# Kernel optimization log

Measured on AMD Instinct MI355X. Metric: run time of the kernel, lower is better.

## Reference

```python
import jax, jax.numpy as jnp
import numpy as np

B, P, EPG = 1000, 100, 1200  # graphs, nodes/graph, edges/graph
IN, HID, OUT, K = 16, 64, 5, 3


def setup_inputs() -> dict:
    key = jax.random.key(0)
    ks = jax.random.split(key, 12)
    offs = jnp.repeat(jnp.arange(B, dtype=jnp.int32) * P, EPG)
    src = jax.random.randint(ks[0], (B * EPG,), 0, P, dtype=jnp.int32) + offs
    dst = jax.random.randint(ks[1], (B * EPG,), 0, P, dtype=jnp.int32) + offs
    graph_ids = jnp.repeat(jnp.arange(B, dtype=jnp.int32), P)
    feat = jax.random.normal(ks[2], (B * P, IN), dtype=jnp.float32)

    def lin(k1, fan_in, fan_out):
        s = 1.0 / np.sqrt(fan_in)
        return jax.random.uniform(k1, (fan_in, fan_out), jnp.float32, -s, s)

    return {
        'feat': feat, 'src': src, 'dst': dst, 'graph_ids': graph_ids,
        'n_graphs': B,
        'W1': lin(ks[3], K * IN, HID), 'b1': jnp.zeros((HID,), jnp.float32),
        'W2': lin(ks[4], K * HID, HID), 'b2': jnp.zeros((HID,), jnp.float32),
        'W3': lin(ks[5], K * HID, HID), 'b3': jnp.zeros((HID,), jnp.float32),
        'Wfc': lin(ks[6], HID, OUT), 'bfc': jnp.zeros((OUT,), jnp.float32),
    }


def _cheb_conv(x, src, dst, d_invsqrt, W, b, k):
    # DGL ChebConv with lambda_max=2 -> re_norm=1, scaled Laplacian = -D^-1/2 A D^-1/2
    n = x.shape[0]

    def Ax(h):
        msg = (h * d_invsqrt)[src]                      # gather from source nodes
        agg = jax.ops.segment_sum(msg, dst, num_segments=n)
        return agg * d_invsqrt

    Xs = [x]
    if k > 1:
        Xs.append(-Ax(Xs[0]))                           # X1 = L_hat X0
        for _ in range(2, k):
            Xs.append(-2.0 * Ax(Xs[-1]) - Xs[-2])       # X_i = 2 L_hat X_{i-1} - X_{i-2}
    Xt = jnp.concatenate(Xs, axis=1)                    # [n, k*f]
    return Xt @ W + b


def reference(feat, src, dst, graph_ids, n_graphs, W1, b1, W2, b2, W3, b3, Wfc, bfc):
    n = feat.shape[0]
    deg = jax.ops.segment_sum(jnp.ones((src.shape[0],), feat.dtype), dst, num_segments=n)
    d_invsqrt = jnp.where(deg < 1.0, 1.0, deg) ** -0.5
    d_invsqrt = d_invsqrt[:, None]

    h = jax.nn.relu(_cheb_conv(feat, src, dst, d_invsqrt, W1, b1, K))
    h = jax.nn.relu(_cheb_conv(h, src, dst, d_invsqrt, W2, b2, K))
    h = jax.nn.relu(_cheb_conv(h, src, dst, d_invsqrt, W3, b3, K))

    # dgl.mean_nodes: per-graph mean pooling
    counts = jax.ops.segment_sum(jnp.ones((n,), h.dtype), graph_ids, num_segments=n_graphs)
    hg = jax.ops.segment_sum(h, graph_ids, num_segments=n_graphs) / counts[:, None]
    return hg @ Wfc + bfc
```

## Files before the change

kernel.cpp:

```cpp
#include <hip/hip_runtime.h>

#define NGRAPH 1000
#define P      100
#define EPG    1200
#define INF    16
#define HID    64
#define NOUT   5


#define FSTR   96
#define T1OFF  64
#define T2OFF  80

#define RK1 64
#define RK2 208
#define L1HI 0
#define L1LO 4096
#define L2HI 8192
#define L2LO 21504
#define L3HI 34816
#define L3LO 48128

typedef short short8 __attribute__((ext_vector_type(8)));
typedef float f32x4  __attribute__((ext_vector_type(4)));

__device__ __forceinline__ int swf(int row, int col) {
    return row * FSTR + (col ^ (((row >> 3) & 3) << 3));
}

__device__ __forceinline__ unsigned packsplit(float x) {
    unsigned u  = __float_as_uint(x);
    unsigned hi = (u + 0x7fffu + ((u >> 16) & 1u)) >> 16;
    float r = x - __uint_as_float(hi << 16);
    unsigned v  = __float_as_uint(r);
    unsigned lo = (v + 0x7fffu + ((v >> 16) & 1u)) >> 16;
    return (hi << 16) | (lo & 0xffffu);
}

__device__ __forceinline__ float up2(short h, short l) {
    return __uint_as_float(((unsigned)(unsigned short)h) << 16) +
           __uint_as_float(((unsigned)(unsigned short)l) << 16);
}

__global__ __launch_bounds__(256) void wprep(
    const float* __restrict__ W1, const float* __restrict__ W2,
    const float* __restrict__ W3, short* __restrict__ wt)
{
    const int i0 = blockIdx.x * blockDim.x + threadIdx.x;
    const int stride = gridDim.x * blockDim.x;
    for (int e = i0; e < HID * RK1; e += stride) {
        int c = e / RK1, r = e % RK1;
        float v = (r < 3 * INF) ? W1[r * HID + c] : 0.f;
        unsigned p = packsplit(v);
        wt[L1HI + e] = (short)(p >> 16);
        wt[L1LO + e] = (short)(p & 0xffffu);
    }
    for (int e = i0; e < HID * RK2; e += stride) {
        int c = e / RK2, r = e % RK2;
        float v2 = (r < 3 * HID) ? W2[r * HID + c] : 0.f;
        float v3 = (r < 3 * HID) ? W3[r * HID + c] : 0.f;
        unsigned p2 = packsplit(v2), p3 = packsplit(v3);
        wt[L2HI + e] = (short)(p2 >> 16); wt[L2LO + e] = (short)(p2 & 0xffffu);
        wt[L3HI + e] = (short)(p3 >> 16); wt[L3LO + e] = (short)(p3 & 0xffffu);
    }
}

template <int SECOND>
__device__ __forceinline__ void dense_prop(
    short* __restrict__ Ahi, short* __restrict__ Alo,
    short8 a00, short8 a01, short8 a02, short8 a03,
    short8 a10, short8 a11, short8 a12, short8 a13,
    bool has2, int srcoff, int dstoff, int ycb,
    int rb0, int rb1, f32x4 dv0, f32x4 dv1, int lane)
{
    const int n16 = lane & 15;
    const int q   = lane >> 4;
    const int kq  = q * 8;
    const int c = (srcoff + n16) ^ (q << 3);
    f32x4 p0, p1;
    p0[0]=0.f; p0[1]=0.f; p0[2]=0.f; p0[3]=0.f;
    p1[0]=0.f; p1[1]=0.f; p1[2]=0.f; p1[3]=0.f;

#define PROPK(KK, A0, A1) { \
    const int b0 = (KK * 32 + kq) * FSTR + c; \
    short8 bhi, blo; \
    if (KK < 3) { \
        bhi[0]=Ahi[b0        ]; blo[0]=Alo[b0        ]; \
        bhi[1]=Ahi[b0+1*FSTR ]; blo[1]=Alo[b0+1*FSTR ]; \
        bhi[2]=Ahi[b0+2*FSTR ]; blo[2]=Alo[b0+2*FSTR ]; \
        bhi[3]=Ahi[b0+3*FSTR ]; blo[3]=Alo[b0+3*FSTR ]; \
        bhi[4]=Ahi[b0+4*FSTR ]; blo[4]=Alo[b0+4*FSTR ]; \
        bhi[5]=Ahi[b0+5*FSTR ]; blo[5]=Alo[b0+5*FSTR ]; \
        bhi[6]=Ahi[b0+6*FSTR ]; blo[6]=Alo[b0+6*FSTR ]; \
        bhi[7]=Ahi[b0+7*FSTR ]; blo[7]=Alo[b0+7*FSTR ]; \
    } else { \
        const int m0 = 96 + kq; \
        const int i0 = (m0+0 < P ? (m0+0)*FSTR : 0) + c; \
        const int i1 = (m0+1 < P ? (m0+1)*FSTR : 0) + c; \
        const int i2 = (m0+2 < P ? (m0+2)*FSTR : 0) + c; \
        const int i3 = (m0+3 < P ? (m0+3)*FSTR : 0) + c; \
        bhi[0]=Ahi[i0]; blo[0]=Alo[i0]; \
        bhi[1]=Ahi[i1]; blo[1]=Alo[i1]; \
        bhi[2]=Ahi[i2]; blo[2]=Alo[i2]; \
        bhi[3]=Ahi[i3]; blo[3]=Alo[i3]; \
        bhi[4]=0; blo[4]=0; \
        bhi[5]=0; blo[5]=0; \
        bhi[6]=0; blo[6]=0; \
        bhi[7]=0; blo[7]=0; \
    } \
    p0 = __builtin_amdgcn_mfma_f32_16x16x32_bf16(A0, bhi, p0, 0, 0, 0); \
    p0 = __builtin_amdgcn_mfma_f32_16x16x32_bf16(A0, blo, p0, 0, 0, 0); \
    if (has2) { \
        p1 = __builtin_amdgcn_mfma_f32_16x16x32_bf16(A1, bhi, p1, 0, 0, 0); \
        p1 = __builtin_amdgcn_mfma_f32_16x16x32_bf16(A1, blo, p1, 0, 0, 0); \
    } }

    PROPK(0, a00, a10)
    PROPK(1, a01, a11)
    PROPK(2, a02, a12)
    PROPK(3, a03, a13)
#undef PROPK

#pragma unroll
    for (int r = 0; r < 4; r++) {
        const int row = rb0 + q * 4 + r;
        const float d2 = dv0[r] * dv0[r];
        float o;
        if (SECOND) {
            const int yi = swf(row, ycb + n16);
            o = -2.f * d2 * p0[r] - up2(Ahi[yi], Alo[yi]);
        } else o = -d2 * p0[r];
        const int di = swf(row, dstoff + n16);
        const unsigned pp = packsplit(o);
        Ahi[di] = (short)(pp >> 16); Alo[di] = (short)pp;
    }
    if (has2) {
#pragma unroll
        for (int r = 0; r < 4; r++) {
            const int row = rb1 + q * 4 + r;
            if (rb1 != 84 || row >= 96) {
                const float d2 = dv1[r] * dv1[r];
                float o;
                if (SECOND) {
                    const int yi = swf(row, ycb + n16);
                    o = -2.f * d2 * p1[r] - up2(Ahi[yi], Alo[yi]);
                } else o = -d2 * p1[r];
                const int di = swf(row, dstoff + n16);
                const unsigned pp = packsplit(o);
                Ahi[di] = (short)(pp >> 16); Alo[di] = (short)pp;
            }
        }
    }
}

template <int F, int FINAL>
__device__ __forceinline__ void cheb_layer(
    short* __restrict__ Ahi, short* __restrict__ Alo,
    const float* __restrict__ dinv,
    short8 a00, short8 a01, short8 a02, short8 a03,
    short8 a10, short8 a11, short8 a12, short8 a13, bool has2,
    const short* __restrict__ whi, const short* __restrict__ wlo,
    const float* __restrict__ bias,
    int tid, int rb0, int rb1, f32x4 dv0, f32x4 dv1)
{
    const int RK   = 3 * F + 16;
    const int lane = tid & 63;
    const int wv   = tid >> 6;
    const int n16  = lane & 15;
    const int q    = lane >> 4;
    const int ncol = (wv << 4) + n16;

    f32x4 acc[7];
#pragma unroll
    for (int t = 0; t < 7; t++) { acc[t][0]=0.f; acc[t][1]=0.f; acc[t][2]=0.f; acc[t][3]=0.f; }

    for (int cb = 0; cb < F; cb += 16) {
        dense_prop<0>(Ahi, Alo, a00,a01,a02,a03, a10,a11,a12,a13, has2,
                      cb,    T1OFF, 0,  rb0, rb1, dv0, dv1, lane);
        __syncthreads();
        dense_prop<1>(Ahi, Alo, a00,a01,a02,a03, a10,a11,a12,a13, has2,
                      T1OFF, T2OFF, cb, rb0, rb1, dv0, dv1, lane);
        __syncthreads();

#pragma unroll
        for (int ks = 0; ks < 2; ks++) {
            int wr, aoff;
            if (ks == 0) {
                wr   = (q == 0) ? cb : (q == 1) ? cb + 8 : (q == 2) ? F + cb : F + cb + 8;
                aoff = (q == 0) ? cb : (q == 1) ? cb + 8 : (q == 2) ? T1OFF  : T1OFF + 8;
            } else {
                wr   = (q == 0) ? 2*F + cb : (q == 1) ? 2*F + cb + 8 : (q == 2) ? 3*F : 3*F + 8;
                aoff = (q == 0) ? T2OFF    : (q == 1) ? T2OFF + 8    : (q == 2) ? T1OFF : T1OFF + 8;
            }
            const short8 bhi = *(const short8*)&whi[ncol * RK + wr];
            const short8 blo = *(const short8*)&wlo[ncol * RK + wr];
#pragma unroll
            for (int t = 0; t < 7; t++) {
                const int row = ((t < 6) ? t * 16 : 84) + n16;
                const int ax  = row * FSTR + (aoff ^ (((row >> 3) & 3) << 3));
                const short8 ahi = *(const short8*)&Ahi[ax];
                const short8 alo = *(const short8*)&Alo[ax];
                acc[t] = __builtin_amdgcn_mfma_f32_16x16x32_bf16(ahi, bhi, acc[t], 0, 0, 0);
                acc[t] = __builtin_amdgcn_mfma_f32_16x16x32_bf16(ahi, blo, acc[t], 0, 0, 0);
                acc[t] = __builtin_amdgcn_mfma_f32_16x16x32_bf16(alo, bhi, acc[t], 0, 0, 0);
            }
        }
        __syncthreads();
    }

    const float bcol = bias[ncol];
#pragma unroll
    for (int t = 0; t < 7; t++) {
        const int rbase = ((t < 6) ? t * 16 : 84) + q * 4;
#pragma unroll
        for (int r = 0; r < 4; r++) {
            const int row = rbase + r;
            if (t < 6 || row >= 96) {
                const float dn = dinv[row];
                const float v = acc[t][r];
                float o;
                if (FINAL) o = fmaxf(v * (1.0f / dn) + bcol, 0.f);
                else       o = fmaxf(v + bcol * dn, 0.f);
                const int oi = swf(row, ncol);
                const unsigned pp = packsplit(o);
                Ahi[oi] = (short)(pp >> 16); Alo[oi] = (short)pp;
            }
        }
    }
    __syncthreads();
}

__global__ __launch_bounds__(256, 4) void gnn_kernel(
    const float* __restrict__ feat,
    const int* __restrict__ src, const int* __restrict__ dst,
    const float* __restrict__ b1, const float* __restrict__ b2,
    const float* __restrict__ b3,
    const float* __restrict__ Wfc, const float* __restrict__ bfc,
    const short* __restrict__ wt,
    float* __restrict__ out)
{
    __shared__ __align__(16) unsigned ldsu[9728];
    __shared__ float meta[128];
    short* Ahi = (short*)ldsu;
    short* Alo = (short*)ldsu + 9600;
    unsigned* cnt = ldsu;

    const int g = blockIdx.x;
    const int tid = threadIdx.x;
    const int base = g * P;
    const int* srcg = src + g * EPG;
    const int* dstg = dst + g * EPG;

    int* deg = (int*)meta;
    for (int i = tid; i < 6400; i += 256) cnt[i] = 0u;
    for (int i = tid; i < P; i += 256) deg[i] = 0;
    __syncthreads();
    for (int e = tid; e < EPG; e += 256) {
        int s = srcg[e] - base;
        int d = dstg[e] - base;
        atomicAdd(&deg[d], 1);
        atomicAdd(&cnt[d * 64 + (s >> 1)], 1u << ((s & 1) * 16));
    }
    __syncthreads();
    for (int i = tid; i < P; i += 256) {
        int dg = deg[i];
        meta[i] = rsqrtf((float)(dg > 1 ? dg : 1));
    }
    const int lane = tid & 63, wv = tid >> 6, q = lane >> 4, n16 = lane & 15;
    const int rb0 = wv * 16;
    const int t2i = wv + 4;
    const int rb1 = (t2i >= 6) ? 84 : t2i * 16;
    const bool has2 = (wv < 3);
    const int arow0 = rb0 + n16;
    const int arow1 = (has2 ? rb1 : rb0) + n16;
    short8 a00, a01, a02, a03, a10, a11, a12, a13;
#define MKA(VAR, AR, KK) { \
    const unsigned w0 = cnt[(AR) * 64 + (KK) * 16 + q * 4 + 0]; \
    const unsigned w1 = cnt[(AR) * 64 + (KK) * 16 + q * 4 + 1]; \
    const unsigned w2 = cnt[(AR) * 64 + (KK) * 16 + q * 4 + 2]; \
    const unsigned w3 = cnt[(AR) * 64 + (KK) * 16 + q * 4 + 3]; \
    short8 t; \
    t[0] = (short)(__float_as_uint((float)(w0 & 0xffffu)) >> 16); \
    t[1] = (short)(__float_as_uint((float)(w0 >> 16))     >> 16); \
    t[2] = (short)(__float_as_uint((float)(w1 & 0xffffu)) >> 16); \
    t[3] = (short)(__float_as_uint((float)(w1 >> 16))     >> 16); \
    t[4] = (short)(__float_as_uint((float)(w2 & 0xffffu)) >> 16); \
    t[5] = (short)(__float_as_uint((float)(w2 >> 16))     >> 16); \
    t[6] = (short)(__float_as_uint((float)(w3 & 0xffffu)) >> 16); \
    t[7] = (short)(__float_as_uint((float)(w3 >> 16))     >> 16); \
    VAR = t; }
    MKA(a00, arow0, 0)  MKA(a01, arow0, 1)  MKA(a02, arow0, 2)  MKA(a03, arow0, 3)
    MKA(a10, arow1, 0)  MKA(a11, arow1, 1)  MKA(a12, arow1, 2)  MKA(a13, arow1, 3)
#undef MKA
    __syncthreads();

    f32x4 dv0, dv1;
#pragma unroll
    for (int r = 0; r < 4; r++) {
        dv0[r] = meta[rb0 + q * 4 + r];
        dv1[r] = meta[(has2 ? rb1 : rb0) + q * 4 + r];
    }
    for (int i = tid; i < P * INF / 4; i += 256) {
        int n = i >> 2, f0 = (i & 3) * 4;
        float4 v = *(const float4*)&feat[(size_t)base * INF + i * 4];
        float dn = meta[n];
        unsigned p0 = packsplit(v.x * dn), p1 = packsplit(v.y * dn);
        unsigned p2 = packsplit(v.z * dn), p3 = packsplit(v.w * dn);
        const int bi = swf(n, f0);
        *(unsigned*)&Ahi[bi]     = (p0 >> 16) | (p1 & 0xffff0000u);
        *(unsigned*)&Ahi[bi + 2] = (p2 >> 16) | (p3 & 0xffff0000u);
        *(unsigned*)&Alo[bi]     = (p0 & 0xffffu) | (p1 << 16);
        *(unsigned*)&Alo[bi + 2] = (p2 & 0xffffu) | (p3 << 16);
    }
    __syncthreads();

    cheb_layer<INF, 0>(Ahi, Alo, meta, a00,a01,a02,a03, a10,a11,a12,a13, has2,
                       wt + L1HI, wt + L1LO, b1, tid, rb0, rb1, dv0, dv1);
    cheb_layer<HID, 0>(Ahi, Alo, meta, a00,a01,a02,a03, a10,a11,a12,a13, has2,
                       wt + L2HI, wt + L2LO, b2, tid, rb0, rb1, dv0, dv1);
    cheb_layer<HID, 1>(Ahi, Alo, meta, a00,a01,a02,a03, a10,a11,a12,a13, has2,
                       wt + L3HI, wt + L3LO, b3, tid, rb0, rb1, dv0, dv1);

    {
        const int l = tid & 63, w = tid >> 6;
        float s = 0.f;
        for (int n = w; n < P; n += 4) {
            const int ii = swf(n, l);
            s += up2(Ahi[ii], Alo[ii]);
        }
        float o0 = s * Wfc[l * NOUT + 0];
        float o1 = s * Wfc[l * NOUT + 1];
        float o2 = s * Wfc[l * NOUT + 2];
        float o3 = s * Wfc[l * NOUT + 3];
        float o4 = s * Wfc[l * NOUT + 4];
#pragma unroll
        for (int d = 1; d < 64; d <<= 1) {
            o0 += __shfl_xor(o0, d);
            o1 += __shfl_xor(o1, d);
            o2 += __shfl_xor(o2, d);
            o3 += __shfl_xor(o3, d);
            o4 += __shfl_xor(o4, d);
        }
        if (l == 0) {
            meta[100 + w * NOUT + 0] = o0;
            meta[100 + w * NOUT + 1] = o1;
            meta[100 + w * NOUT + 2] = o2;
            meta[100 + w * NOUT + 3] = o3;
            meta[100 + w * NOUT + 4] = o4;
        }
    }
    __syncthreads();
    if (tid < NOUT) {
        float o = meta[100 + tid] + meta[105 + tid] + meta[110 + tid] + meta[115 + tid];
        out[g * NOUT + tid] = bfc[tid] + o * (1.0f / P);
    }
}

extern "C" void kernel_launch(void* const* d_in, const int* in_sizes, int n_in,
                              void* d_out, int out_size, void* d_ws, size_t ws_size,
                              hipStream_t stream)
{
    const float* feat = (const float*)d_in[0];
    const int*   src  = (const int*)d_in[1];
    const int*   dst  = (const int*)d_in[2];
    const float* W1  = (const float*)d_in[5];
    const float* b1  = (const float*)d_in[6];
    const float* W2  = (const float*)d_in[7];
    const float* b2  = (const float*)d_in[8];
    const float* W3  = (const float*)d_in[9];
    const float* b3  = (const float*)d_in[10];
    const float* Wfc = (const float*)d_in[11];
    const float* bfc = (const float*)d_in[12];
    float* out = (float*)d_out;

    short* wt = (short*)d_ws;

    wprep<<<64, 256, 0, stream>>>(W1, W2, W3, wt);
    gnn_kernel<<<NGRAPH, 256, 0, stream>>>(feat, src, dst,
                                           b1, b2, b3, Wfc, bfc, wt, out);
}
```

Baseline: 193.1 us.

## Widen LDS feature row stride to 128 with per-row XOR swizzle

The shared-memory feature buffer row stride grows from 96 to 128 shorts, and the XOR swizzle now depends on the low four row bits instead of two bits of row>>3. The propagation B-operand gathers and the dense A-operand loads both go through the new swizzle function. The goal is to remove LDS bank conflicts in the column-wise gathers. The larger LDS footprint lowers the launch-bounds occupancy hint from 4 to 3 blocks per CU.

```diff
diff --git a/kernel.cpp b/kernel.cpp
--- a/kernel.cpp
+++ b/kernel.cpp
@@ -8,7 +8,7 @@
 #define NOUT   5
 
 
-#define FSTR   96
+#define FSTR   128
 #define T1OFF  64
 #define T2OFF  80
 
@@ -25,7 +25,7 @@
 typedef float f32x4  __attribute__((ext_vector_type(4)));
 
 __device__ __forceinline__ int swf(int row, int col) {
-    return row * FSTR + (col ^ (((row >> 3) & 3) << 3));
+    return row * FSTR + (col ^ ((row & 15) << 3));
 }
 
 __device__ __forceinline__ unsigned packsplit(float x) {
@@ -76,37 +76,32 @@
     const int n16 = lane & 15;
     const int q   = lane >> 4;
     const int kq  = q * 8;
-    const int c = (srcoff + n16) ^ (q << 3);
+    const int cc  = srcoff + n16;
     f32x4 p0, p1;
     p0[0]=0.f; p0[1]=0.f; p0[2]=0.f; p0[3]=0.f;
     p1[0]=0.f; p1[1]=0.f; p1[2]=0.f; p1[3]=0.f;
 
 #define PROPK(KK, A0, A1) { \
-    const int b0 = (KK * 32 + kq) * FSTR + c; \
+    const int r0 = KK * 32 + kq; \
     short8 bhi, blo; \
     if (KK < 3) { \
-        bhi[0]=Ahi[b0        ]; blo[0]=Alo[b0        ]; \
-        bhi[1]=Ahi[b0+1*FSTR ]; blo[1]=Alo[b0+1*FSTR ]; \
-        bhi[2]=Ahi[b0+2*FSTR ]; blo[2]=Alo[b0+2*FSTR ]; \
-        bhi[3]=Ahi[b0+3*FSTR ]; blo[3]=Alo[b0+3*FSTR ]; \
-        bhi[4]=Ahi[b0+4*FSTR ]; blo[4]=Alo[b0+4*FSTR ]; \
-        bhi[5]=Ahi[b0+5*FSTR ]; blo[5]=Alo[b0+5*FSTR ]; \
-        bhi[6]=Ahi[b0+6*FSTR ]; blo[6]=Alo[b0+6*FSTR ]; \
-        bhi[7]=Ahi[b0+7*FSTR ]; blo[7]=Alo[b0+7*FSTR ]; \
+        const int i0 = swf(r0 + 0, cc); const int i1 = swf(r0 + 1, cc); \
+        const int i2 = swf(r0 + 2, cc); const int i3 = swf(r0 + 3, cc); \
+        const int i4 = swf(r0 + 4, cc); const int i5 = swf(r0 + 5, cc); \
+        const int i6 = swf(r0 + 6, cc); const int i7 = swf(r0 + 7, cc); \
+        bhi[0]=Ahi[i0]; blo[0]=Alo[i0]; bhi[1]=Ahi[i1]; blo[1]=Alo[i1]; \
+        bhi[2]=Ahi[i2]; blo[2]=Alo[i2]; bhi[3]=Ahi[i3]; blo[3]=Alo[i3]; \
+        bhi[4]=Ahi[i4]; blo[4]=Alo[i4]; bhi[5]=Ahi[i5]; blo[5]=Alo[i5]; \
+        bhi[6]=Ahi[i6]; blo[6]=Alo[i6]; bhi[7]=Ahi[i7]; blo[7]=Alo[i7]; \
     } else { \
-        const int m0 = 96 + kq; \
-        const int i0 = (m0+0 < P ? (m0+0)*FSTR : 0) + c; \
-        const int i1 = (m0+1 < P ? (m0+1)*FSTR : 0) + c; \
-        const int i2 = (m0+2 < P ? (m0+2)*FSTR : 0) + c; \
-        const int i3 = (m0+3 < P ? (m0+3)*FSTR : 0) + c; \
-        bhi[0]=Ahi[i0]; blo[0]=Alo[i0]; \
-        bhi[1]=Ahi[i1]; blo[1]=Alo[i1]; \
-        bhi[2]=Ahi[i2]; blo[2]=Alo[i2]; \
-        bhi[3]=Ahi[i3]; blo[3]=Alo[i3]; \
-        bhi[4]=0; blo[4]=0; \
-        bhi[5]=0; blo[5]=0; \
-        bhi[6]=0; blo[6]=0; \
-        bhi[7]=0; blo[7]=0; \
+        const int i0 = swf((r0 + 0 < P) ? r0 + 0 : 0, cc); \
+        const int i1 = swf((r0 + 1 < P) ? r0 + 1 : 0, cc); \
+        const int i2 = swf((r0 + 2 < P) ? r0 + 2 : 0, cc); \
+        const int i3 = swf((r0 + 3 < P) ? r0 + 3 : 0, cc); \
+        bhi[0]=Ahi[i0]; blo[0]=Alo[i0]; bhi[1]=Ahi[i1]; blo[1]=Alo[i1]; \
+        bhi[2]=Ahi[i2]; blo[2]=Alo[i2]; bhi[3]=Ahi[i3]; blo[3]=Alo[i3]; \
+        bhi[4]=0; blo[4]=0; bhi[5]=0; blo[5]=0; \
+        bhi[6]=0; blo[6]=0; bhi[7]=0; blo[7]=0; \
     } \
     p0 = __builtin_amdgcn_mfma_f32_16x16x32_bf16(A0, bhi, p0, 0, 0, 0); \
     p0 = __builtin_amdgcn_mfma_f32_16x16x32_bf16(A0, blo, p0, 0, 0, 0); \
@@ -197,7 +192,7 @@
 #pragma unroll
             for (int t = 0; t < 7; t++) {
                 const int row = ((t < 6) ? t * 16 : 84) + n16;
-                const int ax  = row * FSTR + (aoff ^ (((row >> 3) & 3) << 3));
+                const int ax  = swf(row, aoff);
                 const short8 ahi = *(const short8*)&Ahi[ax];
                 const short8 alo = *(const short8*)&Alo[ax];
                 acc[t] = __builtin_amdgcn_mfma_f32_16x16x32_bf16(ahi, bhi, acc[t], 0, 0, 0);
@@ -230,7 +225,7 @@
     __syncthreads();
 }
 
-__global__ __launch_bounds__(256, 4) void gnn_kernel(
+__global__ __launch_bounds__(256, 3) void gnn_kernel(
     const float* __restrict__ feat,
     const int* __restrict__ src, const int* __restrict__ dst,
     const float* __restrict__ b1, const float* __restrict__ b2,
@@ -239,10 +234,10 @@
     const short* __restrict__ wt,
     float* __restrict__ out)
 {
-    __shared__ __align__(16) unsigned ldsu[9728];
+    __shared__ __align__(16) unsigned ldsu[12800];
     __shared__ float meta[128];
     short* Ahi = (short*)ldsu;
-    short* Alo = (short*)ldsu + 9600;
+    short* Alo = (short*)ldsu + 12800;
     unsigned* cnt = ldsu;
 
     const int g = blockIdx.x;
```

New measurement: 343.4 us. +77.8%, slower.
